# Kernel optimization log

Hardware: AMD Instinct MI355X
Metric: run time of the kernel (lower is better)

Reference implementation:

```python
import jax, jax.numpy as jnp
import numpy as np

H = 512          # hidden_dim
T = 20           # output_seq_len
EPS = 1e-5


def _ln(x, g, b):
    m = jnp.mean(x, axis=-1, keepdims=True)
    v = jnp.mean((x - m) ** 2, axis=-1, keepdims=True)
    return (x - m) * jax.lax.rsqrt(v + EPS) * g + b


def setup_inputs() -> dict:
    key = jax.random.key(0)
    ks = jax.random.split(key, 20)
    N, LD, PD = 65536, 128, 32
    s = 0.02
    return {
        "z_q": jax.random.normal(ks[0], (N, LD), jnp.float32),
        "f_prior": jax.random.normal(ks[1], (N, PD), jnp.float32),
        # init_mlp: Linear(160 -> 1024) -> LN -> GELU -> Linear(1024 -> 512) -> Tanh
        "W1": jax.random.normal(ks[2], (LD + PD, 2 * H), jnp.float32) * s,
        "b1": jnp.zeros((2 * H,), jnp.float32),
        "g1": jnp.ones((2 * H,), jnp.float32),
        "be1": jnp.zeros((2 * H,), jnp.float32),
        "W2": jax.random.normal(ks[3], (2 * H, H), jnp.float32) * s,
        "b2": jnp.zeros((H,), jnp.float32),
        # start token (output_dim = 1)
        "start_token": jax.random.normal(ks[4], (1,), jnp.float32) * 0.1,
        # GRU, input_size=1, hidden_size=H, gates stacked [r, z, n] (torch layout)
        "W_ih": jax.random.normal(ks[5], (3 * H, 1), jnp.float32) * s,
        "W_hh": jax.random.normal(ks[6], (3 * H, H), jnp.float32) * s,
        "b_ih": jnp.zeros((3 * H,), jnp.float32),
        "b_hh": jnp.zeros((3 * H,), jnp.float32),
        # output_mlp: Linear(H -> H//2) -> LN -> GELU -> Linear(H//2 -> 1)
        "Wo1": jax.random.normal(ks[7], (H, H // 2), jnp.float32) * s,
        "bo1": jnp.zeros((H // 2,), jnp.float32),
        "go": jnp.ones((H // 2,), jnp.float32),
        "beo": jnp.zeros((H // 2,), jnp.float32),
        "Wo2": jax.random.normal(ks[8], (H // 2, 1), jnp.float32) * s,
        "bo2": jnp.zeros((1,), jnp.float32),
    }


def reference(z_q, f_prior, W1, b1, g1, be1, W2, b2, start_token,
              W_ih, W_hh, b_ih, b_hh, Wo1, bo1, go, beo, Wo2, bo2):
    N = z_q.shape[0]
    # init_mlp -> h_0 (dropout is identity at eval)
    combined = jnp.concatenate([z_q, f_prior], axis=1)          # (N, LD+PD)
    h = jnp.tanh(jax.nn.gelu(_ln(combined @ W1 + b1, g1, be1), approximate=False) @ W2 + b2)  # (N, H)

    x0 = jnp.broadcast_to(start_token[None, :], (N, 1))          # (N, 1)

    def step(carry, _):
        h, x = carry
        gi = x @ W_ih.T + b_ih                                   # (N, 3H)
        gh = h @ W_hh.T + b_hh                                   # (N, 3H)
        r = jax.nn.sigmoid(gi[:, :H] + gh[:, :H])
        z = jax.nn.sigmoid(gi[:, H:2 * H] + gh[:, H:2 * H])
        n = jnp.tanh(gi[:, 2 * H:] + r * gh[:, 2 * H:])
        h_new = (1.0 - z) * n + z * h
        y = jax.nn.gelu(_ln(h_new @ Wo1 + bo1, go, beo), approximate=False) @ Wo2 + bo2  # (N, 1)
        return (h_new, y), y

    _, ys = jax.lax.scan(step, (h, x0), None, length=T)          # (T, N, 1)
    preds = jnp.transpose(ys[..., 0], (1, 0))                    # (N, T), output_dim==1 squeeze
    return preds
```

## Files before the change

kernel.cpp:

```cpp
#include <hip/hip_runtime.h>
#include <math.h>


typedef _Float16 f16;
typedef _Float16 f16x4 __attribute__((ext_vector_type(4)));
typedef _Float16 f16x8 __attribute__((ext_vector_type(8)));
typedef float f32x4 __attribute__((ext_vector_type(4)));

#define TSTEPS 20

__device__ __forceinline__ float sigm(float v) { return 1.0f / (1.0f + __expf(-v)); }
__device__ __forceinline__ float tanh_s(float v) {
  float e = __expf(-2.0f * fabsf(v));
  float r = (1.0f - e) / (1.0f + e);
  return copysignf(r, v);
}
__device__ __forceinline__ float gelu_e(float v) {
  return 0.5f * v * (1.0f + erff(v * 0.70710678118654752f));
}
__device__ __forceinline__ void st4(float* d, float4 v) {
  d[0] = v.x; d[1] = v.y; d[2] = v.z; d[3] = v.w;
}

__device__ __forceinline__ int haddr(int buf, int m, int k) {
  return buf + m * 1024 + ((k * 2) ^ ((m & 7) << 4));
}
__device__ __forceinline__ int taddr(int m, int c) {
  return m * 2048 + ((c * 2) ^ ((m & 7) << 4));
}

__global__ void cvt_weights(const float* __restrict__ W1, const float* __restrict__ W2,
                            const float* __restrict__ Whh, const float* __restrict__ Wo1,
                            const float* __restrict__ bih, const float* __restrict__ bhh,
                            f16* __restrict__ w1t, f16* __restrict__ w2t,
                            f16* __restrict__ whh, f16* __restrict__ wo1t,
                            float* __restrict__ bcr, float* __restrict__ bcz) {
  int i = blockIdx.x * 256 + threadIdx.x;
  if (i < 163840) { int n = i / 160; int k = i - n * 160; w1t[i] = (f16)W1[k * 1024 + n]; return; }
  i -= 163840;
  if (i < 524288) { int n = i >> 10; int k = i & 1023; w2t[i] = (f16)W2[k * 512 + n]; return; }
  i -= 524288;
  if (i < 786432) { whh[i] = (f16)Whh[i]; return; }
  i -= 786432;
  if (i < 131072) { int o = i >> 9; int k = i & 511; wo1t[i] = (f16)Wo1[k * 256 + o]; return; }
  i -= 131072;
  if (i < 512) { bcr[i] = bih[i] + bhh[i]; return; }
  i -= 512;
  if (i < 512) { bcz[i] = bih[512 + i] + bhh[512 + i]; return; }
}

__global__ __launch_bounds__(1024, 2)
void gru_main(
    const float* __restrict__ zq, const float* __restrict__ fpr,
    const float* __restrict__ b1, const float* __restrict__ g1, const float* __restrict__ be1,
    const float* __restrict__ b2, const float* __restrict__ stok,
    const float* __restrict__ Wih, const float* __restrict__ bih, const float* __restrict__ bhh,
    const float* __restrict__ bo1, const float* __restrict__ go, const float* __restrict__ beo,
    const float* __restrict__ Wo2, const float* __restrict__ bo2,
    const f16* __restrict__ w1t, const f16* __restrict__ w2t,
    const f16* __restrict__ whh, const f16* __restrict__ wo1t,
    const float* __restrict__ bcr, const float* __restrict__ bcz,
    float* __restrict__ out) {
  __shared__ __align__(16) unsigned char sm[131072];
  __shared__ float sm_s[64 * 20], sm_ss[64 * 20], sm_yp[64 * 20];
  __shared__ float sm_x[64];

  const int tid = threadIdx.x;
  const int w = tid >> 6;
  const int lane = tid & 63;
  const int l16 = lane & 15;
  const int l4 = lane >> 4;
  const int R0 = blockIdx.x * 64;

  const float bo2v = bo2[0];
  if (tid < 64) sm_x[tid] = stok[0];

  #pragma unroll 1
  for (int q = 0; q < 4; ++q) {
    f32x4 acc[4];
    #pragma unroll
    for (int mt = 0; mt < 4; ++mt) acc[mt] = (f32x4){0.f, 0.f, 0.f, 0.f};
    #pragma unroll
    for (int kf = 0; kf < 5; ++kf) {
      const int k0 = kf * 32 + l4 * 8;
      f16x8 B[4];
      #pragma unroll
      for (int mt = 0; mt < 4; ++mt) {
        const int gm = R0 + mt * 16 + l16;
        const float* src = (kf < 4) ? (zq + gm * 128 + k0) : (fpr + gm * 32 + (k0 - 128));
        float4 v0 = *(const float4*)src;
        float4 v1 = *(const float4*)(src + 4);
        f16x8 b;
        b[0] = (f16)v0.x; b[1] = (f16)v0.y; b[2] = (f16)v0.z; b[3] = (f16)v0.w;
        b[4] = (f16)v1.x; b[5] = (f16)v1.y; b[6] = (f16)v1.z; b[7] = (f16)v1.w;
        B[mt] = b;
      }
      const f16x8 A = *(const f16x8*)(w1t + (w * 64 + q * 16 + l16) * 160 + k0);
      #pragma unroll
      for (int mt = 0; mt < 4; ++mt)
        acc[mt] = __builtin_amdgcn_mfma_f32_16x16x32_f16(A, B[mt], acc[mt], 0, 0, 0);
    }
    const int jq = w * 64 + q * 16 + l4 * 4;
    float bb[4]; st4(bb, *(const float4*)(b1 + jq));
    #pragma unroll
    for (int mt = 0; mt < 4; ++mt) {
      f16x4 v;
      #pragma unroll
      for (int r = 0; r < 4; ++r) v[r] = (f16)(acc[mt][r] + bb[r]);
      *(f16x4*)(sm + taddr(mt * 16 + l16, jq)) = v;
    }
  }
  __syncthreads();
  {
    const int m = tid >> 4;
    const int c0 = (tid & 15) * 64;
    float s = 0.f, ss = 0.f;
    #pragma unroll
    for (int cb = 0; cb < 8; ++cb) {
      f16x8 v = *(const f16x8*)(sm + taddr(m, c0 + cb * 8));
      #pragma unroll
      for (int i = 0; i < 8; ++i) { float f = (float)v[i]; s += f; ss += f * f; }
    }
    s += __shfl_xor(s, 1); ss += __shfl_xor(ss, 1);
    s += __shfl_xor(s, 2); ss += __shfl_xor(ss, 2);
    s += __shfl_xor(s, 4); ss += __shfl_xor(ss, 4);
    s += __shfl_xor(s, 8); ss += __shfl_xor(ss, 8);
    const float mean = s * (1.f / 1024.f);
    const float rstd = rsqrtf(ss * (1.f / 1024.f) - mean * mean + 1e-5f);
    #pragma unroll 2
    for (int cb = 0; cb < 8; ++cb) {
      const int c = c0 + cb * 8;
      f16x8 v = *(const f16x8*)(sm + taddr(m, c));
      float4 ga = *(const float4*)(g1 + c);
      float4 gb = *(const float4*)(g1 + c + 4);
      float4 ba = *(const float4*)(be1 + c);
      float4 bb = *(const float4*)(be1 + c + 4);
      float gs[8] = {ga.x, ga.y, ga.z, ga.w, gb.x, gb.y, gb.z, gb.w};
      float bs[8] = {ba.x, ba.y, ba.z, ba.w, bb.x, bb.y, bb.z, bb.w};
      f16x8 o;
      #pragma unroll
      for (int i = 0; i < 8; ++i)
        o[i] = (f16)gelu_e(((float)v[i] - mean) * rstd * gs[i] + bs[i]);
      *(f16x8*)(sm + taddr(m, c)) = o;
    }
  }
  __syncthreads();
  f16x4 h0[2][4];
  #pragma unroll 1
  for (int jh = 0; jh < 2; ++jh) {
    f32x4 acc[4];
    #pragma unroll
    for (int mt = 0; mt < 4; ++mt) acc[mt] = (f32x4){0.f, 0.f, 0.f, 0.f};
    #pragma unroll 2
    for (int kf = 0; kf < 32; ++kf) {
      const int k0 = kf * 32 + l4 * 8;
      f16x8 B[4];
      #pragma unroll
      for (int mt = 0; mt < 4; ++mt)
        B[mt] = *(const f16x8*)(sm + taddr(mt * 16 + l16, k0));
      const f16x8 A = *(const f16x8*)(w2t + (w * 32 + jh * 16 + l16) * 1024 + k0);
      #pragma unroll
      for (int mt = 0; mt < 4; ++mt)
        acc[mt] = __builtin_amdgcn_mfma_f32_16x16x32_f16(A, B[mt], acc[mt], 0, 0, 0);
    }
    const int jq = w * 32 + jh * 16 + l4 * 4;
    float bb[4]; st4(bb, *(const float4*)(b2 + jq));
    #pragma unroll
    for (int mt = 0; mt < 4; ++mt) {
      f16x4 v;
      #pragma unroll
      for (int r = 0; r < 4; ++r) v[r] = (f16)tanh_s(acc[mt][r] + bb[r]);
      h0[jh][mt] = v;
    }
  }
  __syncthreads();
  #pragma unroll
  for (int jh = 0; jh < 2; ++jh) {
    const int jq = w * 32 + jh * 16 + l4 * 4;
    #pragma unroll
    for (int mt = 0; mt < 4; ++mt)
      *(f16x4*)(sm + haddr(0, mt * 16 + l16, jq)) = h0[jh][mt];
  }
  __syncthreads();

  #pragma unroll 1
  for (int t = 0; t < TSTEPS; ++t) {
    const int cur = (t & 1) << 16;
    const int nxt = cur ^ 65536;
    #pragma unroll 1
    for (int q = 0; q < 2; ++q) {
      const int jt = w * 32 + q * 16;
      f32x4 acc[4][3];
      #pragma unroll
      for (int mt = 0; mt < 4; ++mt)
        #pragma unroll
        for (int g = 0; g < 3; ++g) acc[mt][g] = (f32x4){0.f, 0.f, 0.f, 0.f};
      #pragma unroll 2
      for (int kf = 0; kf < 16; ++kf) {
        const int k0 = kf * 32 + l4 * 8;
        f16x8 B[4];
        #pragma unroll
        for (int mt = 0; mt < 4; ++mt)
          B[mt] = *(const f16x8*)(sm + haddr(cur, mt * 16 + l16, k0));
        #pragma unroll
        for (int g = 0; g < 3; ++g) {
          const f16x8 A = *(const f16x8*)(whh + (g * 512 + jt + l16) * 512 + k0);
          #pragma unroll
          for (int mt = 0; mt < 4; ++mt)
            acc[mt][g] = __builtin_amdgcn_mfma_f32_16x16x32_f16(A, B[mt], acc[mt][g], 0, 0, 0);
        }
      }
      if (q == 0) __syncthreads();
      const int jq = jt + l4 * 4;
      float wr[4], wz[4], wn[4], cr[4], cz[4], bn[4], cn[4];
      st4(wr, *(const float4*)(Wih + jq));
      st4(wz, *(const float4*)(Wih + 512 + jq));
      st4(wn, *(const float4*)(Wih + 1024 + jq));
      st4(cr, *(const float4*)(bcr + jq));
      st4(cz, *(const float4*)(bcz + jq));
      st4(bn, *(const float4*)(bih + 1024 + jq));
      st4(cn, *(const float4*)(bhh + 1024 + jq));
      #pragma unroll
      for (int mt = 0; mt < 4; ++mt) {
        const int m = mt * 16 + l16;
        const float x = sm_x[m];
        const int hoff = m * 1024 + ((jq * 2) ^ ((m & 7) << 4));
        const f16x4 ho = *(const f16x4*)(sm + cur + hoff);
        f16x4 hn;
        #pragma unroll
        for (int r = 0; r < 4; ++r) {
          const float gr = sigm(x * wr[r] + cr[r] + acc[mt][0][r]);
          const float gz = sigm(x * wz[r] + cz[r] + acc[mt][1][r]);
          const float gn = tanh_s(x * wn[r] + bn[r] + gr * (acc[mt][2][r] + cn[r]));
          hn[r] = (f16)((1.f - gz) * gn + gz * (float)ho[r]);
        }
        *(f16x4*)(sm + nxt + hoff) = hn;
      }
    }
    __syncthreads();
    {
      f32x4 a2[4];
      #pragma unroll
      for (int mt = 0; mt < 4; ++mt) a2[mt] = (f32x4){0.f, 0.f, 0.f, 0.f};
      #pragma unroll 2
      for (int kf = 0; kf < 16; ++kf) {
        const int k0 = kf * 32 + l4 * 8;
        f16x8 B[4];
        #pragma unroll
        for (int mt = 0; mt < 4; ++mt)
          B[mt] = *(const f16x8*)(sm + haddr(nxt, mt * 16 + l16, k0));
        const f16x8 A = *(const f16x8*)(wo1t + (w * 16 + l16) * 512 + k0);
        #pragma unroll
        for (int mt = 0; mt < 4; ++mt)
          a2[mt] = __builtin_amdgcn_mfma_f32_16x16x32_f16(A, B[mt], a2[mt], 0, 0, 0);
      }
      const int c4 = w * 16 + l4 * 4;
      float vv[4][4];
      float bo1v[4]; st4(bo1v, *(const float4*)(bo1 + c4));
      #pragma unroll
      for (int mt = 0; mt < 4; ++mt) {
        float s = 0.f, ss = 0.f;
        #pragma unroll
        for (int r = 0; r < 4; ++r) {
          const float v = a2[mt][r] + bo1v[r];
          vv[mt][r] = v; s += v; ss += v * v;
        }
        s += __shfl_xor(s, 16); ss += __shfl_xor(ss, 16);
        s += __shfl_xor(s, 32); ss += __shfl_xor(ss, 32);
        if (l4 == 0) {
          const int m = mt * 16 + l16;
          sm_s[m * 20 + w] = s;
          sm_ss[m * 20 + w] = ss;
        }
      }
      __syncthreads();
      float gov[4], bev[4], wv[4];
      st4(gov, *(const float4*)(go + c4));
      st4(bev, *(const float4*)(beo + c4));
      st4(wv, *(const float4*)(Wo2 + c4));
      #pragma unroll
      for (int mt = 0; mt < 4; ++mt) {
        const int m = mt * 16 + l16;
        float s = 0.f, ss = 0.f;
        #pragma unroll
        for (int i = 0; i < 4; ++i) {
          float4 ps = *(const float4*)(sm_s + m * 20 + i * 4);
          float4 pq = *(const float4*)(sm_ss + m * 20 + i * 4);
          s += ps.x + ps.y + ps.z + ps.w;
          ss += pq.x + pq.y + pq.z + pq.w;
        }
        const float mean = s * (1.f / 256.f);
        const float rstd = rsqrtf(ss * (1.f / 256.f) - mean * mean + 1e-5f);
        float y = 0.f;
        #pragma unroll
        for (int r = 0; r < 4; ++r)
          y += gelu_e((vv[mt][r] - mean) * rstd * gov[r] + bev[r]) * wv[r];
        y += __shfl_xor(y, 16);
        y += __shfl_xor(y, 32);
        if (l4 == 0) sm_yp[m * 20 + w] = y;
      }
      __syncthreads();
      if (tid < 64) {
        const int m = tid;
        float y = bo2v;
        #pragma unroll
        for (int i = 0; i < 4; ++i) {
          float4 ps = *(const float4*)(sm_yp + m * 20 + i * 4);
          y += ps.x + ps.y + ps.z + ps.w;
        }
        sm_x[m] = y;
        out[(R0 + m) * 20 + t] = y;
      }
    }
  }
}

extern "C" void kernel_launch(void* const* d_in, const int* in_sizes, int n_in,
                              void* d_out, int out_size, void* d_ws, size_t ws_size,
                              hipStream_t stream) {
  const float* zq   = (const float*)d_in[0];
  const float* fpr  = (const float*)d_in[1];
  const float* W1   = (const float*)d_in[2];
  const float* b1   = (const float*)d_in[3];
  const float* g1   = (const float*)d_in[4];
  const float* be1  = (const float*)d_in[5];
  const float* W2   = (const float*)d_in[6];
  const float* b2   = (const float*)d_in[7];
  const float* stok = (const float*)d_in[8];
  const float* Wih  = (const float*)d_in[9];
  const float* Whh  = (const float*)d_in[10];
  const float* bih  = (const float*)d_in[11];
  const float* bhh  = (const float*)d_in[12];
  const float* Wo1  = (const float*)d_in[13];
  const float* bo1  = (const float*)d_in[14];
  const float* go   = (const float*)d_in[15];
  const float* beo  = (const float*)d_in[16];
  const float* Wo2  = (const float*)d_in[17];
  const float* bo2  = (const float*)d_in[18];

  char* ws = (char*)d_ws;
  f16* w1t   = (f16*)(ws + 0);
  f16* w2t   = (f16*)(ws + 327680);
  f16* whh   = (f16*)(ws + 1376256);
  f16* wo1t  = (f16*)(ws + 2949120);
  float* bcr = (float*)(ws + 3211264);
  float* bcz = (float*)(ws + 3213312);

  cvt_weights<<<6276, 256, 0, stream>>>(W1, W2, Whh, Wo1, bih, bhh,
                                        w1t, w2t, whh, wo1t, bcr, bcz);

  const int N = in_sizes[0] / 128;
  gru_main<<<N / 64, 1024, 0, stream>>>(zq, fpr, b1, g1, be1, b2, stok, Wih, bih, bhh,
                                        bo1, go, beo, Wo2, bo2, w1t, w2t, whh, wo1t,
                                        bcr, bcz, (float*)d_out);
}
```

Before: 5.215 ms.

## Halve block to 512 threads and use MFMA-fragment-native LDS layout

Blocks shrink from 16 to 8 waves, and each wave now covers twice as many output columns per phase. Each wave's weight fragment is reused across more MFMAs and the cross-wave LayerNorm reductions have fewer partials. Hidden and activation tiles in LDS move from row-major XOR-swizzled storage to a fragment-ordered layout, so each lane reads its B operand as one contiguous 16-byte chunk at lane*16. The cost is higher register pressure (24 accumulators per wave in the GRU step) and fewer waves available to hide latency.

```diff
diff --git a/kernel.cpp b/kernel.cpp
--- a/kernel.cpp
+++ b/kernel.cpp
@@ -22,11 +22,8 @@
   d[0] = v.x; d[1] = v.y; d[2] = v.z; d[3] = v.w;
 }
 
-__device__ __forceinline__ int haddr(int buf, int m, int k) {
-  return buf + m * 1024 + ((k * 2) ^ ((m & 7) << 4));
-}
-__device__ __forceinline__ int taddr(int m, int c) {
-  return m * 2048 + ((c * 2) ^ ((m & 7) << 4));
+__device__ __forceinline__ int fa(int m, int k) {
+  return (((k >> 5) * 4 + (m >> 4)) << 10) + (((m & 15) + ((k >> 3) & 3) * 16) << 4) + ((k & 7) * 2);
 }
 
 __global__ void cvt_weights(const float* __restrict__ W1, const float* __restrict__ W2,
@@ -49,7 +46,7 @@
   if (i < 512) { bcz[i] = bih[512 + i] + bhh[512 + i]; return; }
 }
 
-__global__ __launch_bounds__(1024, 2)
+__global__ __launch_bounds__(512, 2)
 void gru_main(
     const float* __restrict__ zq, const float* __restrict__ fpr,
     const float* __restrict__ b1, const float* __restrict__ g1, const float* __restrict__ be1,
@@ -62,7 +59,7 @@
     const float* __restrict__ bcr, const float* __restrict__ bcz,
     float* __restrict__ out) {
   __shared__ __align__(16) unsigned char sm[131072];
-  __shared__ float sm_s[64 * 20], sm_ss[64 * 20], sm_yp[64 * 20];
+  __shared__ float sm_s[256], sm_ss[256], sm_yp[256];
   __shared__ float sm_x[64];
 
   const int tid = threadIdx.x;
@@ -76,61 +73,69 @@
   if (tid < 64) sm_x[tid] = stok[0];
 
   #pragma unroll 1
-  for (int q = 0; q < 4; ++q) {
-    f32x4 acc[4];
-    #pragma unroll
-    for (int mt = 0; mt < 4; ++mt) acc[mt] = (f32x4){0.f, 0.f, 0.f, 0.f};
-    #pragma unroll
-    for (int kf = 0; kf < 5; ++kf) {
-      const int k0 = kf * 32 + l4 * 8;
-      f16x8 B[4];
+  for (int p = 0; p < 4; ++p) {
+    #pragma unroll 1
+    for (int jh = 0; jh < 2; ++jh) {
+      const int jq0 = w * 128 + p * 32 + jh * 16;
+      f32x4 acc[4];
+      #pragma unroll
+      for (int mt = 0; mt < 4; ++mt) acc[mt] = (f32x4){0.f, 0.f, 0.f, 0.f};
+      #pragma unroll
+      for (int kf = 0; kf < 5; ++kf) {
+        const int k0 = kf * 32 + l4 * 8;
+        f16x8 B[4];
+        #pragma unroll
+        for (int mt = 0; mt < 4; ++mt) {
+          const int gm = R0 + mt * 16 + l16;
+          const float* src = (kf < 4) ? (zq + gm * 128 + k0) : (fpr + gm * 32 + (k0 - 128));
+          float4 v0 = *(const float4*)src;
+          float4 v1 = *(const float4*)(src + 4);
+          f16x8 b;
+          b[0] = (f16)v0.x; b[1] = (f16)v0.y; b[2] = (f16)v0.z; b[3] = (f16)v0.w;
+          b[4] = (f16)v1.x; b[5] = (f16)v1.y; b[6] = (f16)v1.z; b[7] = (f16)v1.w;
+          B[mt] = b;
+        }
+        const f16x8 A = *(const f16x8*)(w1t + (jq0 + l16) * 160 + k0);
+        #pragma unroll
+        for (int mt = 0; mt < 4; ++mt)
+          acc[mt] = __builtin_amdgcn_mfma_f32_16x16x32_f16(A, B[mt], acc[mt], 0, 0, 0);
+      }
+      const int jq = jq0 + l4 * 4;
+      float bb[4]; st4(bb, *(const float4*)(b1 + jq));
       #pragma unroll
       for (int mt = 0; mt < 4; ++mt) {
-        const int gm = R0 + mt * 16 + l16;
-        const float* src = (kf < 4) ? (zq + gm * 128 + k0) : (fpr + gm * 32 + (k0 - 128));
-        float4 v0 = *(const float4*)src;
-        float4 v1 = *(const float4*)(src + 4);
-        f16x8 b;
-        b[0] = (f16)v0.x; b[1] = (f16)v0.y; b[2] = (f16)v0.z; b[3] = (f16)v0.w;
-        b[4] = (f16)v1.x; b[5] = (f16)v1.y; b[6] = (f16)v1.z; b[7] = (f16)v1.w;
-        B[mt] = b;
-      }
-      const f16x8 A = *(const f16x8*)(w1t + (w * 64 + q * 16 + l16) * 160 + k0);
-      #pragma unroll
-      for (int mt = 0; mt < 4; ++mt)
-        acc[mt] = __builtin_amdgcn_mfma_f32_16x16x32_f16(A, B[mt], acc[mt], 0, 0, 0);
-    }
-    const int jq = w * 64 + q * 16 + l4 * 4;
-    float bb[4]; st4(bb, *(const float4*)(b1 + jq));
-    #pragma unroll
-    for (int mt = 0; mt < 4; ++mt) {
-      f16x4 v;
-      #pragma unroll
-      for (int r = 0; r < 4; ++r) v[r] = (f16)(acc[mt][r] + bb[r]);
-      *(f16x4*)(sm + taddr(mt * 16 + l16, jq)) = v;
+        f16x4 v;
+        #pragma unroll
+        for (int r = 0; r < 4; ++r) v[r] = (f16)(acc[mt][r] + bb[r]);
+        *(f16x4*)(sm + fa(mt * 16 + l16, jq)) = v;
+      }
     }
   }
   __syncthreads();
   {
-    const int m = tid >> 4;
-    const int c0 = (tid & 15) * 64;
+    const int mt = w & 3, half = w >> 2;
+    const int row = mt * 16 + l16;
     float s = 0.f, ss = 0.f;
-    #pragma unroll
-    for (int cb = 0; cb < 8; ++cb) {
-      f16x8 v = *(const f16x8*)(sm + taddr(m, c0 + cb * 8));
+    #pragma unroll 4
+    for (int it = 0; it < 16; ++it) {
+      const int kb = half * 16 + it;
+      f16x8 v = *(const f16x8*)(sm + (kb * 4 + mt) * 1024 + lane * 16);
       #pragma unroll
       for (int i = 0; i < 8; ++i) { float f = (float)v[i]; s += f; ss += f * f; }
     }
-    s += __shfl_xor(s, 1); ss += __shfl_xor(ss, 1);
-    s += __shfl_xor(s, 2); ss += __shfl_xor(ss, 2);
-    s += __shfl_xor(s, 4); ss += __shfl_xor(ss, 4);
-    s += __shfl_xor(s, 8); ss += __shfl_xor(ss, 8);
-    const float mean = s * (1.f / 1024.f);
-    const float rstd = rsqrtf(ss * (1.f / 1024.f) - mean * mean + 1e-5f);
+    s += __shfl_xor(s, 16); ss += __shfl_xor(ss, 16);
+    s += __shfl_xor(s, 32); ss += __shfl_xor(ss, 32);
+    if (l4 == 0) { sm_s[row * 2 + half] = s; sm_ss[row * 2 + half] = ss; }
+    __syncthreads();
+    const float mean = (sm_s[row * 2] + sm_s[row * 2 + 1]) * (1.f / 1024.f);
+    const float q2 = (sm_ss[row * 2] + sm_ss[row * 2 + 1]) * (1.f / 1024.f);
+    const float rstd = rsqrtf(q2 - mean * mean + 1e-5f);
     #pragma unroll 2
-    for (int cb = 0; cb < 8; ++cb) {
-      const int c = c0 + cb * 8;
-      f16x8 v = *(const f16x8*)(sm + taddr(m, c));
+    for (int it = 0; it < 16; ++it) {
+      const int kb = half * 16 + it;
+      const int off = (kb * 4 + mt) * 1024 + lane * 16;
+      const int c = kb * 32 + l4 * 8;
+      f16x8 v = *(const f16x8*)(sm + off);
       float4 ga = *(const float4*)(g1 + c);
       float4 gb = *(const float4*)(g1 + c + 4);
       float4 ba = *(const float4*)(be1 + c);
@@ -141,45 +146,45 @@
       #pragma unroll
       for (int i = 0; i < 8; ++i)
         o[i] = (f16)gelu_e(((float)v[i] - mean) * rstd * gs[i] + bs[i]);
-      *(f16x8*)(sm + taddr(m, c)) = o;
+      *(f16x8*)(sm + off) = o;
     }
   }
   __syncthreads();
-  f16x4 h0[2][4];
+  f16x4 hold[4][4];
   #pragma unroll 1
-  for (int jh = 0; jh < 2; ++jh) {
+  for (int pp = 0; pp < 4; ++pp) {
+    const int jq0 = w * 64 + pp * 16;
     f32x4 acc[4];
     #pragma unroll
     for (int mt = 0; mt < 4; ++mt) acc[mt] = (f32x4){0.f, 0.f, 0.f, 0.f};
     #pragma unroll 2
     for (int kf = 0; kf < 32; ++kf) {
-      const int k0 = kf * 32 + l4 * 8;
       f16x8 B[4];
       #pragma unroll
       for (int mt = 0; mt < 4; ++mt)
-        B[mt] = *(const f16x8*)(sm + taddr(mt * 16 + l16, k0));
-      const f16x8 A = *(const f16x8*)(w2t + (w * 32 + jh * 16 + l16) * 1024 + k0);
+        B[mt] = *(const f16x8*)(sm + (kf * 4 + mt) * 1024 + lane * 16);
+      const f16x8 A = *(const f16x8*)(w2t + (jq0 + l16) * 1024 + kf * 32 + l4 * 8);
       #pragma unroll
       for (int mt = 0; mt < 4; ++mt)
         acc[mt] = __builtin_amdgcn_mfma_f32_16x16x32_f16(A, B[mt], acc[mt], 0, 0, 0);
     }
-    const int jq = w * 32 + jh * 16 + l4 * 4;
+    const int jq = jq0 + l4 * 4;
     float bb[4]; st4(bb, *(const float4*)(b2 + jq));
     #pragma unroll
     for (int mt = 0; mt < 4; ++mt) {
       f16x4 v;
       #pragma unroll
       for (int r = 0; r < 4; ++r) v[r] = (f16)tanh_s(acc[mt][r] + bb[r]);
-      h0[jh][mt] = v;
+      hold[pp][mt] = v;
     }
   }
   __syncthreads();
   #pragma unroll
-  for (int jh = 0; jh < 2; ++jh) {
-    const int jq = w * 32 + jh * 16 + l4 * 4;
+  for (int pp = 0; pp < 4; ++pp) {
+    const int jq = w * 64 + pp * 16 + l4 * 4;
     #pragma unroll
     for (int mt = 0; mt < 4; ++mt)
-      *(f16x4*)(sm + haddr(0, mt * 16 + l16, jq)) = h0[jh][mt];
+      *(f16x4*)(sm + fa(mt * 16 + l16, jq)) = hold[pp][mt];
   }
   __syncthreads();
 
@@ -188,128 +193,138 @@
     const int cur = (t & 1) << 16;
     const int nxt = cur ^ 65536;
     #pragma unroll 1
-    for (int q = 0; q < 2; ++q) {
-      const int jt = w * 32 + q * 16;
-      f32x4 acc[4][3];
+    for (int p = 0; p < 2; ++p) {
+      f32x4 acc[4][3][2];
       #pragma unroll
       for (int mt = 0; mt < 4; ++mt)
         #pragma unroll
-        for (int g = 0; g < 3; ++g) acc[mt][g] = (f32x4){0.f, 0.f, 0.f, 0.f};
+        for (int g = 0; g < 3; ++g)
+          #pragma unroll
+          for (int jh = 0; jh < 2; ++jh) acc[mt][g][jh] = (f32x4){0.f, 0.f, 0.f, 0.f};
       #pragma unroll 2
       for (int kf = 0; kf < 16; ++kf) {
-        const int k0 = kf * 32 + l4 * 8;
         f16x8 B[4];
         #pragma unroll
         for (int mt = 0; mt < 4; ++mt)
-          B[mt] = *(const f16x8*)(sm + haddr(cur, mt * 16 + l16, k0));
-        #pragma unroll
-        for (int g = 0; g < 3; ++g) {
-          const f16x8 A = *(const f16x8*)(whh + (g * 512 + jt + l16) * 512 + k0);
-          #pragma unroll
-          for (int mt = 0; mt < 4; ++mt)
-            acc[mt][g] = __builtin_amdgcn_mfma_f32_16x16x32_f16(A, B[mt], acc[mt][g], 0, 0, 0);
+          B[mt] = *(const f16x8*)(sm + cur + (kf * 4 + mt) * 1024 + lane * 16);
+        #pragma unroll
+        for (int g = 0; g < 3; ++g)
+          #pragma unroll
+          for (int jh = 0; jh < 2; ++jh) {
+            const f16x8 A = *(const f16x8*)(whh + (g * 512 + w * 64 + p * 32 + jh * 16 + l16) * 512 + kf * 32 + l4 * 8);
+            #pragma unroll
+            for (int mt = 0; mt < 4; ++mt)
+              acc[mt][g][jh] = __builtin_amdgcn_mfma_f32_16x16x32_f16(A, B[mt], acc[mt][g][jh], 0, 0, 0);
+          }
+      }
+      if (p == 0) __syncthreads();
+      #pragma unroll
+      for (int jh = 0; jh < 2; ++jh) {
+        const int jq = w * 64 + p * 32 + jh * 16 + l4 * 4;
+        float wr[4], wz[4], wn[4], cr[4], cz[4], bn[4], cn[4];
+        st4(wr, *(const float4*)(Wih + jq));
+        st4(wz, *(const float4*)(Wih + 512 + jq));
+        st4(wn, *(const float4*)(Wih + 1024 + jq));
+        st4(cr, *(const float4*)(bcr + jq));
+        st4(cz, *(const float4*)(bcz + jq));
+        st4(bn, *(const float4*)(bih + 1024 + jq));
+        st4(cn, *(const float4*)(bhh + 1024 + jq));
+        #pragma unroll
+        for (int mt = 0; mt < 4; ++mt) {
+          const int m = mt * 16 + l16;
+          const float x = sm_x[m];
+          const int hoff = fa(m, jq);
+          const f16x4 ho = *(const f16x4*)(sm + cur + hoff);
+          f16x4 hn;
+          #pragma unroll
+          for (int r = 0; r < 4; ++r) {
+            const float gr = sigm(x * wr[r] + cr[r] + acc[mt][0][jh][r]);
+            const float gz = sigm(x * wz[r] + cz[r] + acc[mt][1][jh][r]);
+            const float gn = tanh_s(x * wn[r] + bn[r] + gr * (acc[mt][2][jh][r] + cn[r]));
+            hn[r] = (f16)((1.f - gz) * gn + gz * (float)ho[r]);
+          }
+          *(f16x4*)(sm + nxt + hoff) = hn;
         }
-      }
-      if (q == 0) __syncthreads();
-      const int jq = jt + l4 * 4;
-      float wr[4], wz[4], wn[4], cr[4], cz[4], bn[4], cn[4];
-      st4(wr, *(const float4*)(Wih + jq));
-      st4(wz, *(const float4*)(Wih + 512 + jq));
-      st4(wn, *(const float4*)(Wih + 1024 + jq));
-      st4(cr, *(const float4*)(bcr + jq));
-      st4(cz, *(const float4*)(bcz + jq));
-      st4(bn, *(const float4*)(bih + 1024 + jq));
-      st4(cn, *(const float4*)(bhh + 1024 + jq));
-      #pragma unroll
-      for (int mt = 0; mt < 4; ++mt) {
-        const int m = mt * 16 + l16;
-        const float x = sm_x[m];
-        const int hoff = m * 1024 + ((jq * 2) ^ ((m & 7) << 4));
-        const f16x4 ho = *(const f16x4*)(sm + cur + hoff);
-        f16x4 hn;
-        #pragma unroll
-        for (int r = 0; r < 4; ++r) {
-          const float gr = sigm(x * wr[r] + cr[r] + acc[mt][0][r]);
-          const float gz = sigm(x * wz[r] + cz[r] + acc[mt][1][r]);
-          const float gn = tanh_s(x * wn[r] + bn[r] + gr * (acc[mt][2][r] + cn[r]));
-          hn[r] = (f16)((1.f - gz) * gn + gz * (float)ho[r]);
-        }
-        *(f16x4*)(sm + nxt + hoff) = hn;
       }
     }
     __syncthreads();
     {
-      f32x4 a2[4];
-      #pragma unroll
-      for (int mt = 0; mt < 4; ++mt) a2[mt] = (f32x4){0.f, 0.f, 0.f, 0.f};
+      const int mg = w >> 2, jg = w & 3;
+      f32x4 a2[2][4];
+      #pragma unroll
+      for (int mi = 0; mi < 2; ++mi)
+        #pragma unroll
+        for (int jt2 = 0; jt2 < 4; ++jt2) a2[mi][jt2] = (f32x4){0.f, 0.f, 0.f, 0.f};
       #pragma unroll 2
       for (int kf = 0; kf < 16; ++kf) {
-        const int k0 = kf * 32 + l4 * 8;
-        f16x8 B[4];
-        #pragma unroll
-        for (int mt = 0; mt < 4; ++mt)
-          B[mt] = *(const f16x8*)(sm + haddr(nxt, mt * 16 + l16, k0));
-        const f16x8 A = *(const f16x8*)(wo1t + (w * 16 + l16) * 512 + k0);
-        #pragma unroll
-        for (int mt = 0; mt < 4; ++mt)
-          a2[mt] = __builtin_amdgcn_mfma_f32_16x16x32_f16(A, B[mt], a2[mt], 0, 0, 0);
-      }
-      const int c4 = w * 16 + l4 * 4;
-      float vv[4][4];
-      float bo1v[4]; st4(bo1v, *(const float4*)(bo1 + c4));
-      #pragma unroll
-      for (int mt = 0; mt < 4; ++mt) {
+        f16x8 B[2];
+        #pragma unroll
+        for (int mi = 0; mi < 2; ++mi)
+          B[mi] = *(const f16x8*)(sm + nxt + (kf * 4 + mg * 2 + mi) * 1024 + lane * 16);
+        #pragma unroll
+        for (int jt2 = 0; jt2 < 4; ++jt2) {
+          const f16x8 A = *(const f16x8*)(wo1t + (jg * 64 + jt2 * 16 + l16) * 512 + kf * 32 + l4 * 8);
+          #pragma unroll
+          for (int mi = 0; mi < 2; ++mi)
+            a2[mi][jt2] = __builtin_amdgcn_mfma_f32_16x16x32_f16(A, B[mi], a2[mi][jt2], 0, 0, 0);
+        }
+      }
+      float vv[2][4][4];
+      float bo1v[4][4];
+      #pragma unroll
+      for (int jt2 = 0; jt2 < 4; ++jt2)
+        st4(bo1v[jt2], *(const float4*)(bo1 + jg * 64 + jt2 * 16 + l4 * 4));
+      #pragma unroll
+      for (int mi = 0; mi < 2; ++mi) {
         float s = 0.f, ss = 0.f;
         #pragma unroll
-        for (int r = 0; r < 4; ++r) {
-          const float v = a2[mt][r] + bo1v[r];
-          vv[mt][r] = v; s += v; ss += v * v;
-        }
+        for (int jt2 = 0; jt2 < 4; ++jt2)
+          #pragma unroll
+          for (int r = 0; r < 4; ++r) {
+            const float v = a2[mi][jt2][r] + bo1v[jt2][r];
+            vv[mi][jt2][r] = v; s += v; ss += v * v;
+          }
         s += __shfl_xor(s, 16); ss += __shfl_xor(ss, 16);
         s += __shfl_xor(s, 32); ss += __shfl_xor(ss, 32);
         if (l4 == 0) {
-          const int m = mt * 16 + l16;
-          sm_s[m * 20 + w] = s;
-          sm_ss[m * 20 + w] = ss;
+          const int m = (mg * 2 + mi) * 16 + l16;
+          sm_s[m * 4 + jg] = s;
+          sm_ss[m * 4 + jg] = ss;
         }
       }
       __syncthreads();
-      float gov[4], bev[4], wv[4];
-      st4(gov, *(const float4*)(go + c4));
-      st4(bev, *(const float4*)(beo + c4));
-      st4(wv, *(const float4*)(Wo2 + c4));
-      #pragma unroll
-      for (int mt = 0; mt < 4; ++mt) {
-        const int m = mt * 16 + l16;
-        float s = 0.f, ss = 0.f;
-        #pragma unroll
-        for (int i = 0; i < 4; ++i) {
-          float4 ps = *(const float4*)(sm_s + m * 20 + i * 4);
-          float4 pq = *(const float4*)(sm_ss + m * 20 + i * 4);
-          s += ps.x + ps.y + ps.z + ps.w;
-          ss += pq.x + pq.y + pq.z + pq.w;
-        }
-        const float mean = s * (1.f / 256.f);
-        const float rstd = rsqrtf(ss * (1.f / 256.f) - mean * mean + 1e-5f);
+      float gov[4][4], bev[4][4], wv[4][4];
+      #pragma unroll
+      for (int jt2 = 0; jt2 < 4; ++jt2) {
+        const int jb = jg * 64 + jt2 * 16 + l4 * 4;
+        st4(gov[jt2], *(const float4*)(go + jb));
+        st4(bev[jt2], *(const float4*)(beo + jb));
+        st4(wv[jt2], *(const float4*)(Wo2 + jb));
+      }
+      #pragma unroll
+      for (int mi = 0; mi < 2; ++mi) {
+        const int m = (mg * 2 + mi) * 16 + l16;
+        float4 ps = *(const float4*)(sm_s + m * 4);
+        float4 pq = *(const float4*)(sm_ss + m * 4);
+        const float mean = (ps.x + ps.y + ps.z + ps.w) * (1.f / 256.f);
+        const float q2 = (pq.x + pq.y + pq.z + pq.w) * (1.f / 256.f);
+        const float rstd = rsqrtf(q2 - mean * mean + 1e-5f);
         float y = 0.f;
         #pragma unroll
-        for (int r = 0; r < 4; ++r)
-          y += gelu_e((vv[mt][r] - mean) * rstd * gov[r] + bev[r]) * wv[r];
+        for (int jt2 = 0; jt2 < 4; ++jt2)
+          #pragma unroll
+          for (int r = 0; r < 4; ++r)
+            y += gelu_e((vv[mi][jt2][r] - mean) * rstd * gov[jt2][r] + bev[jt2][r]) * wv[jt2][r];
         y += __shfl_xor(y, 16);
         y += __shfl_xor(y, 32);
-        if (l4 == 0) sm_yp[m * 20 + w] = y;
+        if (l4 == 0) sm_yp[m * 4 + jg] = y;
       }
       __syncthreads();
       if (tid < 64) {
-        const int m = tid;
-        float y = bo2v;
-        #pragma unroll
-        for (int i = 0; i < 4; ++i) {
-          float4 ps = *(const float4*)(sm_yp + m * 20 + i * 4);
-          y += ps.x + ps.y + ps.z + ps.w;
-        }
-        sm_x[m] = y;
-        out[(R0 + m) * 20 + t] = y;
+        float4 ps = *(const float4*)(sm_yp + tid * 4);
+        const float y = bo2v + ps.x + ps.y + ps.z + ps.w;
+        sm_x[tid] = y;
+        out[(R0 + tid) * 20 + t] = y;
       }
     }
   }
@@ -350,7 +365,7 @@
                                         w1t, w2t, whh, wo1t, bcr, bcz);
 
   const int N = in_sizes[0] / 128;
-  gru_main<<<N / 64, 1024, 0, stream>>>(zq, fpr, b1, g1, be1, b2, stok, Wih, bih, bhh,
-                                        bo1, go, beo, Wo2, bo2, w1t, w2t, whh, wo1t,
-                                        bcr, bcz, (float*)d_out);
-}
+  gru_main<<<N / 64, 512, 0, stream>>>(zq, fpr, b1, g1, be1, b2, stok, Wih, bih, bhh,
+                                       bo1, go, beo, Wo2, bo2, w1t, w2t, whh, wo1t,
+                                       bcr, bcz, (float*)d_out);
+}
```

After: 5.997 ms. 15.0% more time.
